# Kernel tuning notes

Hardware: AMD Instinct MI355X
Metric: run time of the kernel (lower is better)

The kernel has to match this reference:

```python
import jax, jax.numpy as jnp
import numpy as np

N_HEADS = 16


def setup_inputs() -> dict:
    key = jax.random.key(0)
    ks = jax.random.split(key, 7)
    B, S, D = 2, 2048, 1024
    x = jax.random.normal(ks[0], (B, S, D), dtype=jnp.float32)
    attn_mask = jax.random.normal(ks[1], (S, S), dtype=jnp.float32) * 0.1
    attn_bias = jax.random.normal(ks[2], (B, S, S), dtype=jnp.float32) * 0.1
    Wqkv = jax.random.normal(ks[3], (D, 3 * D), dtype=jnp.float32) * (D ** -0.5)
    bqkv = jnp.zeros((3 * D,), dtype=jnp.float32)
    Wout = jax.random.normal(ks[4], (D, D), dtype=jnp.float32) * (D ** -0.5)
    bout = jnp.zeros((D,), dtype=jnp.float32)
    return {"x": x, "attn_mask": attn_mask, "attn_bias": attn_bias,
            "Wqkv": Wqkv, "bqkv": bqkv, "Wout": Wout, "bout": bout}


def reference(x, attn_mask, attn_bias, Wqkv, bqkv, Wout, bout):
    B, S, D = x.shape
    H = N_HEADS
    hd = D // H
    # qkv projection: [B,S,3D] -> [3,B,H,S,hd]
    qkv = (x @ Wqkv + bqkv).reshape(B, S, 3, H, hd).transpose(2, 0, 3, 1, 4)
    q, k, v = qkv[0], qkv[1], qkv[2]
    scores = jnp.einsum('bhqd,bhkd->bhqk', q, k) / (hd ** 0.5)
    scores = scores + attn_mask[None, None, :, :] + attn_bias[:, None, :, :]
    attn = jax.nn.softmax(scores, axis=-1)  # dropout p=0.0 (eval)
    out = jnp.einsum('bhqk,bhkd->bhqd', attn, v)
    out = out.transpose(0, 2, 1, 3).reshape(B, S, D)
    return out @ Wout + bout
```

## Files before the change

### kernel.cpp

```cpp
#include <hip/hip_runtime.h>
#include <hip/hip_bf16.h>


#define S_LEN 2048
#define DMODEL 1024
#define NH 16
#define HD 64

typedef __bf16 bf16x8 __attribute__((ext_vector_type(8)));
typedef __bf16 bf16x4 __attribute__((ext_vector_type(4)));
typedef __bf16 bf16x2v __attribute__((ext_vector_type(2)));
typedef float f32x4 __attribute__((ext_vector_type(4)));
typedef short s16x4 __attribute__((ext_vector_type(4)));

#define GLD_LDS16(g, l)                                              \
  __builtin_amdgcn_global_load_lds(                                  \
      (const __attribute__((address_space(1))) unsigned int*)(g),    \
      (__attribute__((address_space(3))) unsigned int*)(l), 16, 0, 0)

#if __has_builtin(__builtin_amdgcn_mfma_f32_16x16x16bf16_1k)
#define HAVE_MFMA_16x16x16_BF16 1
#else
#define HAVE_MFMA_16x16x16_BF16 0
#endif

#if __has_builtin(__builtin_amdgcn_exp2f)
#define EXP2F(x) __builtin_amdgcn_exp2f(x)
#else
static __device__ __forceinline__ float EXP2F(float x) {
  float r;
  asm volatile("v_exp_f32 %0, %1" : "=v"(r) : "v"(x));
  return r;
}
#endif

#define LOG2E 1.44269504f

__global__ __launch_bounds__(256) void cvt_x(const float* __restrict__ X,
                                             __bf16* __restrict__ Xb) {
  int i = blockIdx.x * 256 + threadIdx.x;
  float4 v = ((const float4*)X)[i];
  bf16x4 o = {(__bf16)v.x, (__bf16)v.y, (__bf16)v.z, (__bf16)v.w};
  *(bf16x4*)&Xb[(size_t)i * 4] = o;
}

__global__ __launch_bounds__(256) void cvt_wt(const float* __restrict__ W,
                                              __bf16* __restrict__ Wt,
                                              int ncols) {
  __shared__ float tile[64][65];
  const int n0 = blockIdx.x * 64;
  const int k0 = blockIdx.y * 64;
  const int tid = threadIdx.x;
  {
    int c = tid & 63, r4 = tid >> 6;
#pragma unroll
    for (int p = 0; p < 16; ++p) {
      int r = r4 + p * 4;
      tile[r][c] = W[(size_t)(k0 + r) * ncols + n0 + c];
    }
  }
  __syncthreads();
  {
    int cc = (tid & 31) * 2, r8 = tid >> 5;
#pragma unroll
    for (int p = 0; p < 8; ++p) {
      int rr = r8 + p * 8;
      bf16x2v o = {(__bf16)tile[cc][rr], (__bf16)tile[cc + 1][rr]};
      *(bf16x2v*)&Wt[(size_t)(n0 + rr) * 1024 + k0 + cc] = o;
    }
  }
}

__global__ __launch_bounds__(256) void mb_fuse(const float* __restrict__ mask,
                                               const float* __restrict__ bias,
                                               __bf16* __restrict__ MB) {
  const int kt = blockIdx.x, qt = blockIdx.y, b = blockIdx.z;
  const int tid = threadIdx.x;
  __shared__ __bf16 sm[64][68];
  {
    const int r0 = tid >> 4;
    const int cc = (tid & 15) * 4;
    const float* mrow = mask + (size_t)(qt * 64) * S_LEN + kt * 64;
    const float* brow =
        bias + ((size_t)b * S_LEN + qt * 64) * S_LEN + kt * 64;
#pragma unroll
    for (int p = 0; p < 4; ++p) {
      int r = r0 + p * 16;
      float4 m = *(const float4*)(mrow + (size_t)r * S_LEN + cc);
      float4 a = *(const float4*)(brow + (size_t)r * S_LEN + cc);
      sm[r][cc + 0] = (__bf16)((m.x + a.x) * LOG2E);
      sm[r][cc + 1] = (__bf16)((m.y + a.y) * LOG2E);
      sm[r][cc + 2] = (__bf16)((m.z + a.z) * LOG2E);
      sm[r][cc + 3] = (__bf16)((m.w + a.w) * LOG2E);
    }
  }
  __syncthreads();
  const int w = tid >> 6, lane = tid & 63;
  const int quad = lane >> 4, cl = lane & 15;
  __bf16 vals[16];
#pragma unroll
  for (int ct = 0; ct < 4; ++ct) {
    bf16x4 v = *(const bf16x4*)&sm[w * 16 + cl][ct * 16 + quad * 4];
    *(bf16x4*)&vals[ct * 4] = v;
  }
  __bf16* op =
      MB + (((size_t)(b * 32 + qt) * 32 + kt) * 4096) + (w * 64 + lane) * 16;
  *(bf16x8*)op = *(bf16x8*)&vals[0];
  *(bf16x8*)(op + 8) = *(bf16x8*)&vals[8];
}

__global__ __launch_bounds__(256) void gemm_qkv_mfma(
    const __bf16* __restrict__ Xb, const __bf16* __restrict__ Wt,
    const float* __restrict__ bqkv, __bf16* __restrict__ Qb,
    __bf16* __restrict__ Kb, __bf16* __restrict__ Vtb) {
  __shared__ __align__(16) __bf16 As[128 * 32];
  __shared__ __align__(16) __bf16 Bs[128 * 32];
  const int tid = threadIdx.x;
  const int w = tid >> 6, lane = tid & 63;
  const int c = lane & 15, quad = lane >> 4;
  const int wm = w >> 1, wn = w & 1;
  const int rowBase = blockIdx.y * 128;
  const int colBase = blockIdx.x * 128;

  f32x4 acc[4][4] = {};

  const __bf16* gA0 =
      Xb + (size_t)(rowBase + w * 32 + (lane >> 2)) * 1024 + (lane & 3) * 8;
  const __bf16* gB0 =
      Wt + (size_t)(colBase + w * 32 + (lane >> 2)) * 1024 + (lane & 3) * 8;
  __bf16* lA0 = &As[(w * 32) * 32];
  __bf16* lB0 = &Bs[(w * 32) * 32];

  for (int k0 = 0; k0 < 1024; k0 += 32) {
    __syncthreads();
#pragma unroll
    for (int p = 0; p < 2; ++p) {
      GLD_LDS16(gA0 + (size_t)p * 16 * 1024 + k0, lA0 + p * 16 * 32);
      GLD_LDS16(gB0 + (size_t)p * 16 * 1024 + k0, lB0 + p * 16 * 32);
    }
    __syncthreads();

    bf16x8 af[4], bfr[4];
#pragma unroll
    for (int mt = 0; mt < 4; ++mt)
      af[mt] = *(const bf16x8*)&As[(wm * 64 + mt * 16 + c) * 32 + quad * 8];
#pragma unroll
    for (int nt = 0; nt < 4; ++nt)
      bfr[nt] = *(const bf16x8*)&Bs[(wn * 64 + nt * 16 + c) * 32 + quad * 8];
#pragma unroll
    for (int mt = 0; mt < 4; ++mt)
#pragma unroll
      for (int nt = 0; nt < 4; ++nt)
        acc[mt][nt] = __builtin_amdgcn_mfma_f32_16x16x32_bf16(
            af[mt], bfr[nt], acc[mt][nt], 0, 0, 0);
  }

#pragma unroll
  for (int mt = 0; mt < 4; ++mt) {
    int row0 = rowBase + wm * 64 + mt * 16 + quad * 4;
#pragma unroll
    for (int nt = 0; nt < 4; ++nt) {
      int col = colBase + wn * 64 + nt * 16 + c;
      float bias = bqkv[col];
      int three = col >> 10;
      int h = (col & 1023) >> 6;
      int d = col & 63;
#pragma unroll
      for (int r = 0; r < 4; ++r) {
        int rr = row0 + r;
        int bb = rr >> 11, s = rr & 2047;
        float val = acc[mt][nt][r] + bias;
        size_t ho = (size_t)(bb * NH + h);
        if (three == 0)
          Qb[(ho * S_LEN + s) * HD + d] = (__bf16)val;
        else if (three == 1)
          Kb[(ho * S_LEN + s) * HD + d] = (__bf16)val;
        else
          Vtb[(ho * HD + d) * S_LEN + s] = (__bf16)val;
      }
    }
  }
}

__global__ __launch_bounds__(256) void attn_mfma(
    const __bf16* __restrict__ Qb, const __bf16* __restrict__ Kb,
    const __bf16* __restrict__ Vtb, const __bf16* __restrict__ MB,
    __bf16* __restrict__ AOb) {
  const int qt = blockIdx.x, h = blockIdx.y, b = blockIdx.z;
  const int tid = threadIdx.x;
  const int w = tid >> 6;
  const int lane = tid & 63;
  const int c = lane & 15;
  const int quad = lane >> 4;

  __shared__ __align__(16) __bf16 Ks[2][64 * 64];
  __shared__ __align__(16) __bf16 Vs[2][64 * 64];
#if !HAVE_MFMA_16x16x16_BF16
  __shared__ __align__(16) __bf16 P2[4][16 * 72];
#endif

  const size_t headoff = (size_t)(b * NH + h) * S_LEN * HD;
  const __bf16* Qg = Qb + headoff + (size_t)(qt * 128) * HD;
  const __bf16* Kg = Kb + headoff;
  const __bf16* Vg = Vtb + headoff;
  const __bf16* MBq0 =
      MB + ((size_t)(b * 32 + qt * 2 + 0) * 32) * 4096 + (w * 64 + lane) * 16;
  const __bf16* MBq1 =
      MB + ((size_t)(b * 32 + qt * 2 + 1) * 32) * 4096 + (w * 64 + lane) * 16;

  const int f0 = tid >> 3, f1 = f0 + 32;
  const int j = tid & 7;
  const int sj0 = j ^ (f0 & 7);
  const int sj1 = j ^ (f1 & 7);
  const int lds0 = tid * 8;
  const int lds1 = (256 + tid) * 8;

  bf16x8 qa[2][2];
#pragma unroll
  for (int g = 0; g < 2; ++g) {
    qa[g][0] = *(const bf16x8*)(Qg + (g * 64 + w * 16 + c) * HD + quad * 8);
    qa[g][1] =
        *(const bf16x8*)(Qg + (g * 64 + w * 16 + c) * HD + quad * 8 + 32);
  }

  const int rs0 = (quad ^ (c & 7)) * 8;
  const int rs1 = ((quad + 4) ^ (c & 7)) * 8;

  f32x4 Oa[2][4] = {};
  f32x4 psum[2] = {};

  GLD_LDS16(Kg + (size_t)f0 * HD + sj0 * 8, &Ks[0][lds0]);
  GLD_LDS16(Kg + (size_t)f1 * HD + sj1 * 8, &Ks[0][lds1]);
  GLD_LDS16(Vg + (size_t)f0 * S_LEN + sj0 * 8, &Vs[0][lds0]);
  GLD_LDS16(Vg + (size_t)f1 * S_LEN + sj1 * 8, &Vs[0][lds1]);

  const __bf16* kgp0 = Kg + (size_t)(64 + f0) * HD + sj0 * 8;
  const __bf16* kgp1 = Kg + (size_t)(64 + f1) * HD + sj1 * 8;
  const __bf16* vgp0 = Vg + (size_t)f0 * S_LEN + 64 + sj0 * 8;
  const __bf16* vgp1 = Vg + (size_t)f1 * S_LEN + 64 + sj1 * 8;

  bf16x8 rMB[2][2];
  rMB[0][0] = *(const bf16x8*)MBq0;
  rMB[0][1] = *(const bf16x8*)(MBq0 + 8);
  rMB[1][0] = *(const bf16x8*)MBq1;
  rMB[1][1] = *(const bf16x8*)(MBq1 + 8);

  __syncthreads();

  const float c1 = 0.125f * LOG2E;

#pragma unroll 2
  for (int kt = 0; kt < 32; ++kt) {
    const int cur = kt & 1, nxt = cur ^ 1;
    bf16x8 nMB[2][2];
    {
      const __bf16* m0 = MBq0 + (size_t)(kt + 1) * 4096;
      const __bf16* m1 = MBq1 + (size_t)(kt + 1) * 4096;
      nMB[0][0] = *(const bf16x8*)m0;
      nMB[0][1] = *(const bf16x8*)(m0 + 8);
      nMB[1][0] = *(const bf16x8*)m1;
      nMB[1][1] = *(const bf16x8*)(m1 + 8);
    }
    if (kt < 31) {
      GLD_LDS16(kgp0, &Ks[nxt][lds0]);
      GLD_LDS16(kgp1, &Ks[nxt][lds1]);
      GLD_LDS16(vgp0, &Vs[nxt][lds0]);
      GLD_LDS16(vgp1, &Vs[nxt][lds1]);
    }
    kgp0 += 64 * HD;
    kgp1 += 64 * HD;
    vgp0 += 64;
    vgp1 += 64;

    bf16x8 kf0[4], kf1[4];
#pragma unroll
    for (int ct = 0; ct < 4; ++ct) {
      kf0[ct] = *(const bf16x8*)&Ks[cur][(ct * 16 + c) * 64 + rs0];
      kf1[ct] = *(const bf16x8*)&Ks[cur][(ct * 16 + c) * 64 + rs1];
    }

    f32x4 sv[2][4];
    __builtin_amdgcn_s_setprio(1);
#pragma unroll
    for (int g = 0; g < 2; ++g)
#pragma unroll
      for (int ct = 0; ct < 4; ++ct) {
        f32x4 a = {};
        a = __builtin_amdgcn_mfma_f32_16x16x32_bf16(kf0[ct], qa[g][0], a, 0,
                                                    0, 0);
        a = __builtin_amdgcn_mfma_f32_16x16x32_bf16(kf1[ct], qa[g][1], a, 0,
                                                    0, 0);
        sv[g][ct] = a;
      }
    __builtin_amdgcn_s_setprio(0);

#if HAVE_MFMA_16x16x16_BF16
    s16x4 vf[4][4];
#pragma unroll
    for (int ft = 0; ft < 4; ++ft) {
      const int fr = ft * 16 + c;
#pragma unroll
      for (int ct = 0; ct < 4; ++ct) {
        const int chunk = ((ct * 2 + (quad >> 1)) ^ (fr & 7)) * 8 +
                          (quad & 1) * 4;
        vf[ft][ct] = *(const s16x4*)&Vs[cur][fr * 64 + chunk];
      }
    }
#endif

    s16x4 pb[2][4];
#pragma unroll
    for (int g = 0; g < 2; ++g)
#pragma unroll
      for (int ct = 0; ct < 4; ++ct) {
        f32x4 pv;
#pragma unroll
        for (int r = 0; r < 4; ++r) {
          float mb = (ct < 2) ? (float)rMB[g][0][ct * 4 + r]
                              : (float)rMB[g][1][(ct - 2) * 4 + r];
          pv[r] = EXP2F(sv[g][ct][r] * c1 + mb);
        }
        psum[g] += pv;
        __bf16 t4[4];
#pragma unroll
        for (int r = 0; r < 4; ++r) t4[r] = (__bf16)pv[r];
        pb[g][ct] = *(s16x4*)t4;
      }
#pragma unroll
    for (int g = 0; g < 2; ++g) {
      rMB[g][0] = nMB[g][0];
      rMB[g][1] = nMB[g][1];
    }

#if HAVE_MFMA_16x16x16_BF16
    __builtin_amdgcn_s_setprio(1);
#pragma unroll
    for (int g = 0; g < 2; ++g)
#pragma unroll
      for (int ft = 0; ft < 4; ++ft)
#pragma unroll
        for (int ct = 0; ct < 4; ++ct)
          Oa[g][ft] = __builtin_amdgcn_mfma_f32_16x16x16bf16_1k(
              vf[ft][ct], pb[g][ct], Oa[g][ft], 0, 0, 0);
    __builtin_amdgcn_s_setprio(0);
#else
#pragma unroll
    for (int g = 0; g < 2; ++g) {
#pragma unroll
      for (int ct = 0; ct < 4; ++ct)
        *(bf16x4*)&P2[w][c * 72 + ct * 16 + quad * 4] = *(bf16x4*)&pb[g][ct];
      bf16x8 pf0 = *(const bf16x8*)&P2[w][c * 72 + quad * 8];
      bf16x8 pf1 = *(const bf16x8*)&P2[w][c * 72 + 32 + quad * 8];
#pragma unroll
      for (int ft = 0; ft < 4; ++ft) {
        const int fr = ft * 16 + c;
        bf16x8 vf0 = *(const bf16x8*)&Vs[cur][fr * 64 + rs0];
        bf16x8 vf1 = *(const bf16x8*)&Vs[cur][fr * 64 + rs1];
        Oa[g][ft] = __builtin_amdgcn_mfma_f32_16x16x32_bf16(vf0, pf0,
                                                            Oa[g][ft], 0, 0, 0);
        Oa[g][ft] = __builtin_amdgcn_mfma_f32_16x16x32_bf16(vf1, pf1,
                                                            Oa[g][ft], 0, 0, 0);
      }
    }
#endif

    __syncthreads();
  }
#pragma unroll
  for (int g = 0; g < 2; ++g) {
    float lsum = psum[g][0] + psum[g][1] + psum[g][2] + psum[g][3];
    lsum += __shfl_xor(lsum, 16);
    lsum += __shfl_xor(lsum, 32);
    const float invl = 1.0f / lsum;
    __bf16* orow = AOb +
                   (size_t)(b * S_LEN + qt * 128 + g * 64 + w * 16 + c) *
                       DMODEL +
                   h * HD;
#pragma unroll
    for (int ft = 0; ft < 4; ++ft) {
      __bf16 t4[4];
#pragma unroll
      for (int r = 0; r < 4; ++r) t4[r] = (__bf16)(Oa[g][ft][r] * invl);
      *(bf16x4*)(orow + ft * 16 + quad * 4) = *(bf16x4*)t4;
    }
  }
}

__global__ __launch_bounds__(256) void gemm_out_mfma(
    const __bf16* __restrict__ AOb, const __bf16* __restrict__ Wt2,
    const float* __restrict__ bout, float* __restrict__ Out) {
  __shared__ __align__(16) __bf16 As[128 * 32];
  __shared__ __align__(16) __bf16 Bs[64 * 32];
  const int tid = threadIdx.x;
  const int w = tid >> 6, lane = tid & 63;
  const int c = lane & 15, quad = lane >> 4;
  const int rowBase = blockIdx.y * 128;
  const int colBase = blockIdx.x * 64;

  f32x4 acc[2][4] = {};

  const __bf16* gA0 =
      AOb + (size_t)(rowBase + w * 32 + (lane >> 2)) * 1024 + (lane & 3) * 8;
  const __bf16* gB0 =
      Wt2 + (size_t)(colBase + w * 16 + (lane >> 2)) * 1024 + (lane & 3) * 8;
  __bf16* lA0 = &As[(w * 32) * 32];
  __bf16* lB0 = &Bs[(w * 16) * 32];

  for (int k0 = 0; k0 < 1024; k0 += 32) {
    __syncthreads();
#pragma unroll
    for (int p = 0; p < 2; ++p)
      GLD_LDS16(gA0 + (size_t)p * 16 * 1024 + k0, lA0 + p * 16 * 32);
    GLD_LDS16(gB0 + k0, lB0);
    __syncthreads();

    bf16x8 af[2], bfr[4];
#pragma unroll
    for (int mt = 0; mt < 2; ++mt)
      af[mt] = *(const bf16x8*)&As[(w * 32 + mt * 16 + c) * 32 + quad * 8];
#pragma unroll
    for (int nt = 0; nt < 4; ++nt)
      bfr[nt] = *(const bf16x8*)&Bs[(nt * 16 + c) * 32 + quad * 8];
#pragma unroll
    for (int mt = 0; mt < 2; ++mt)
#pragma unroll
      for (int nt = 0; nt < 4; ++nt)
        acc[mt][nt] = __builtin_amdgcn_mfma_f32_16x16x32_bf16(
            af[mt], bfr[nt], acc[mt][nt], 0, 0, 0);
  }

#pragma unroll
  for (int mt = 0; mt < 2; ++mt) {
    int row0 = rowBase + w * 32 + mt * 16 + quad * 4;
#pragma unroll
    for (int nt = 0; nt < 4; ++nt) {
      int col = colBase + nt * 16 + c;
      float bias = bout[col];
#pragma unroll
      for (int r = 0; r < 4; ++r)
        Out[(size_t)(row0 + r) * 1024 + col] = acc[mt][nt][r] + bias;
    }
  }
}

extern "C" void kernel_launch(void* const* d_in, const int* in_sizes, int n_in,
                              void* d_out, int out_size, void* d_ws,
                              size_t ws_size, hipStream_t stream) {
  const float* x = (const float*)d_in[0];
  const float* attn_mask = (const float*)d_in[1];
  const float* attn_bias = (const float*)d_in[2];
  const float* Wqkv = (const float*)d_in[3];
  const float* bqkv = (const float*)d_in[4];
  const float* Wout = (const float*)d_in[5];
  const float* bout = (const float*)d_in[6];
  float* out = (float*)d_out;

  __bf16* base = (__bf16*)d_ws;
  __bf16* Xb = base;
  __bf16* AOb = base;
  __bf16* Wt = base + 4194304;
  __bf16* Qb = base + 8388608;
  __bf16* Kb = base + 12582912;
  __bf16* Vtb = base + 16777216;
  __bf16* MB = base + 20971520;
  __bf16* Wt2 = base + 29360128;

  cvt_x<<<4096, 256, 0, stream>>>(x, Xb);
  cvt_wt<<<dim3(48, 16), 256, 0, stream>>>(Wqkv, Wt, 3072);
  cvt_wt<<<dim3(16, 16), 256, 0, stream>>>(Wout, Wt2, 1024);
  mb_fuse<<<dim3(32, 32, 2), 256, 0, stream>>>(attn_mask, attn_bias, MB);
  gemm_qkv_mfma<<<dim3(24, 32), 256, 0, stream>>>(Xb, Wt, bqkv, Qb, Kb, Vtb);
  attn_mfma<<<dim3(16, NH, 2), 256, 0, stream>>>(Qb, Kb, Vtb, MB, AOb);
  gemm_out_mfma<<<dim3(16, 32), 256, 0, stream>>>(AOb, Wt2, bout, out);
}
```

Baseline: 273.3 us.

## Split attention key range across two blocks and merge preprocessing launches

The attention kernel now splits the 32 key tiles into two halves handled by separate blocks. This doubles the grid so more of the GPU's compute units are occupied. Each half writes unnormalized bf16 partial outputs and row sums, and a new combine kernel adds the halves and normalizes them. Separately, the conversion kernels for x, both weights and mask+bias are fused into one preprocess launch to cut launch overhead. The split adds an extra global round trip for the partial outputs. It also reuses workspace regions and the output buffer as scratch.

```diff
diff --git a/kernel.cpp b/kernel.cpp
--- a/kernel.cpp
+++ b/kernel.cpp
@@ -36,77 +36,88 @@
 
 #define LOG2E 1.44269504f
 
-__global__ __launch_bounds__(256) void cvt_x(const float* __restrict__ X,
-                                             __bf16* __restrict__ Xb) {
-  int i = blockIdx.x * 256 + threadIdx.x;
-  float4 v = ((const float4*)X)[i];
-  bf16x4 o = {(__bf16)v.x, (__bf16)v.y, (__bf16)v.z, (__bf16)v.w};
-  *(bf16x4*)&Xb[(size_t)i * 4] = o;
-}
-
-__global__ __launch_bounds__(256) void cvt_wt(const float* __restrict__ W,
-                                              __bf16* __restrict__ Wt,
-                                              int ncols) {
-  __shared__ float tile[64][65];
-  const int n0 = blockIdx.x * 64;
-  const int k0 = blockIdx.y * 64;
+__global__ __launch_bounds__(256) void preprocess(
+    const float* __restrict__ x, const float* __restrict__ mask,
+    const float* __restrict__ bias, const float* __restrict__ Wqkv,
+    const float* __restrict__ Wout, __bf16* __restrict__ Xb,
+    __bf16* __restrict__ Wt, __bf16* __restrict__ Wt2,
+    __bf16* __restrict__ MB) {
+  __shared__ __align__(16) char smem[64 * 65 * 4];
+  const int bid = blockIdx.x;
   const int tid = threadIdx.x;
-  {
-    int c = tid & 63, r4 = tid >> 6;
-#pragma unroll
-    for (int p = 0; p < 16; ++p) {
-      int r = r4 + p * 4;
-      tile[r][c] = W[(size_t)(k0 + r) * ncols + n0 + c];
-    }
-  }
-  __syncthreads();
-  {
-    int cc = (tid & 31) * 2, r8 = tid >> 5;
-#pragma unroll
-    for (int p = 0; p < 8; ++p) {
-      int rr = r8 + p * 8;
-      bf16x2v o = {(__bf16)tile[cc][rr], (__bf16)tile[cc + 1][rr]};
-      *(bf16x2v*)&Wt[(size_t)(n0 + rr) * 1024 + k0 + cc] = o;
-    }
-  }
-}
-
-__global__ __launch_bounds__(256) void mb_fuse(const float* __restrict__ mask,
-                                               const float* __restrict__ bias,
-                                               __bf16* __restrict__ MB) {
-  const int kt = blockIdx.x, qt = blockIdx.y, b = blockIdx.z;
-  const int tid = threadIdx.x;
-  __shared__ __bf16 sm[64][68];
-  {
-    const int r0 = tid >> 4;
-    const int cc = (tid & 15) * 4;
-    const float* mrow = mask + (size_t)(qt * 64) * S_LEN + kt * 64;
-    const float* brow =
-        bias + ((size_t)b * S_LEN + qt * 64) * S_LEN + kt * 64;
-#pragma unroll
-    for (int p = 0; p < 4; ++p) {
-      int r = r0 + p * 16;
-      float4 m = *(const float4*)(mrow + (size_t)r * S_LEN + cc);
-      float4 a = *(const float4*)(brow + (size_t)r * S_LEN + cc);
-      sm[r][cc + 0] = (__bf16)((m.x + a.x) * LOG2E);
-      sm[r][cc + 1] = (__bf16)((m.y + a.y) * LOG2E);
-      sm[r][cc + 2] = (__bf16)((m.z + a.z) * LOG2E);
-      sm[r][cc + 3] = (__bf16)((m.w + a.w) * LOG2E);
-    }
-  }
-  __syncthreads();
-  const int w = tid >> 6, lane = tid & 63;
-  const int quad = lane >> 4, cl = lane & 15;
-  __bf16 vals[16];
-#pragma unroll
-  for (int ct = 0; ct < 4; ++ct) {
-    bf16x4 v = *(const bf16x4*)&sm[w * 16 + cl][ct * 16 + quad * 4];
-    *(bf16x4*)&vals[ct * 4] = v;
-  }
-  __bf16* op =
-      MB + (((size_t)(b * 32 + qt) * 32 + kt) * 4096) + (w * 64 + lane) * 16;
-  *(bf16x8*)op = *(bf16x8*)&vals[0];
-  *(bf16x8*)(op + 8) = *(bf16x8*)&vals[8];
+
+  if (bid < 4096) {
+    int i = bid * 256 + tid;
+    float4 v = ((const float4*)x)[i];
+    bf16x4 o = {(__bf16)v.x, (__bf16)v.y, (__bf16)v.z, (__bf16)v.w};
+    *(bf16x4*)&Xb[(size_t)i * 4] = o;
+  } else if (bid < 5120) {
+    const float* W;
+    __bf16* Wo;
+    int ncols, n0, k0;
+    if (bid < 4864) {
+      int id = bid - 4096;
+      W = Wqkv; Wo = Wt; ncols = 3072;
+      n0 = (id % 48) * 64; k0 = (id / 48) * 64;
+    } else {
+      int id = bid - 4864;
+      W = Wout; Wo = Wt2; ncols = 1024;
+      n0 = (id & 15) * 64; k0 = (id >> 4) * 64;
+    }
+    float(*tile)[65] = (float(*)[65])smem;
+    {
+      int c = tid & 63, r4 = tid >> 6;
+#pragma unroll
+      for (int p = 0; p < 16; ++p) {
+        int r = r4 + p * 4;
+        tile[r][c] = W[(size_t)(k0 + r) * ncols + n0 + c];
+      }
+    }
+    __syncthreads();
+    {
+      int cc = (tid & 31) * 2, r8 = tid >> 5;
+#pragma unroll
+      for (int p = 0; p < 8; ++p) {
+        int rr = r8 + p * 8;
+        bf16x2v o = {(__bf16)tile[cc][rr], (__bf16)tile[cc + 1][rr]};
+        *(bf16x2v*)&Wo[(size_t)(n0 + rr) * 1024 + k0 + cc] = o;
+      }
+    }
+  } else {
+    int id = bid - 5120;
+    const int kt = id & 31, qt = (id >> 5) & 31, b = id >> 10;
+    __bf16(*sm)[68] = (__bf16(*)[68])smem;
+    {
+      const int r0 = tid >> 4;
+      const int cc = (tid & 15) * 4;
+      const float* mrow = mask + (size_t)(qt * 64) * S_LEN + kt * 64;
+      const float* brow =
+          bias + ((size_t)b * S_LEN + qt * 64) * S_LEN + kt * 64;
+#pragma unroll
+      for (int p = 0; p < 4; ++p) {
+        int r = r0 + p * 16;
+        float4 m = *(const float4*)(mrow + (size_t)r * S_LEN + cc);
+        float4 a = *(const float4*)(brow + (size_t)r * S_LEN + cc);
+        sm[r][cc + 0] = (__bf16)((m.x + a.x) * LOG2E);
+        sm[r][cc + 1] = (__bf16)((m.y + a.y) * LOG2E);
+        sm[r][cc + 2] = (__bf16)((m.z + a.z) * LOG2E);
+        sm[r][cc + 3] = (__bf16)((m.w + a.w) * LOG2E);
+      }
+    }
+    __syncthreads();
+    const int w = tid >> 6, lane = tid & 63;
+    const int quad = lane >> 4, cl = lane & 15;
+    __bf16 vals[16];
+#pragma unroll
+    for (int ct = 0; ct < 4; ++ct) {
+      bf16x4 v = *(const bf16x4*)&sm[w * 16 + cl][ct * 16 + quad * 4];
+      *(bf16x4*)&vals[ct * 4] = v;
+    }
+    __bf16* op =
+        MB + (((size_t)(b * 32 + qt) * 32 + kt) * 4096) + (w * 64 + lane) * 16;
+    *(bf16x8*)op = *(bf16x8*)&vals[0];
+    *(bf16x8*)(op + 8) = *(bf16x8*)&vals[8];
+  }
 }
 
 __global__ __launch_bounds__(256) void gemm_qkv_mfma(
@@ -185,8 +196,10 @@
 __global__ __launch_bounds__(256) void attn_mfma(
     const __bf16* __restrict__ Qb, const __bf16* __restrict__ Kb,
     const __bf16* __restrict__ Vtb, const __bf16* __restrict__ MB,
-    __bf16* __restrict__ AOb) {
-  const int qt = blockIdx.x, h = blockIdx.y, b = blockIdx.z;
+    __bf16* __restrict__ PO, float* __restrict__ L) {
+  const int qt = blockIdx.x, h = blockIdx.y;
+  const int b = blockIdx.z >> 1, half = blockIdx.z & 1;
+  const int kt0 = half * 16;
   const int tid = threadIdx.x;
   const int w = tid >> 6;
   const int lane = tid & 63;
@@ -203,10 +216,13 @@
   const __bf16* Qg = Qb + headoff + (size_t)(qt * 128) * HD;
   const __bf16* Kg = Kb + headoff;
   const __bf16* Vg = Vtb + headoff;
-  const __bf16* MBq0 =
-      MB + ((size_t)(b * 32 + qt * 2 + 0) * 32) * 4096 + (w * 64 + lane) * 16;
-  const __bf16* MBq1 =
-      MB + ((size_t)(b * 32 + qt * 2 + 1) * 32) * 4096 + (w * 64 + lane) * 16;
+  const __bf16* MBq0 = MB + ((size_t)(b * 32 + qt * 2 + 0) * 32 + kt0) * 4096 +
+                       (w * 64 + lane) * 16;
+  const __bf16* MBq1 = MB + ((size_t)(b * 32 + qt * 2 + 1) * 32 + kt0) * 4096 +
+                       (w * 64 + lane) * 16;
+
+  __bf16* POx = PO + (size_t)half * 4194304;
+  float* Lx = L + half * 65536;
 
   const int f0 = tid >> 3, f1 = f0 + 32;
   const int j = tid & 7;
@@ -229,15 +245,16 @@
   f32x4 Oa[2][4] = {};
   f32x4 psum[2] = {};
 
-  GLD_LDS16(Kg + (size_t)f0 * HD + sj0 * 8, &Ks[0][lds0]);
-  GLD_LDS16(Kg + (size_t)f1 * HD + sj1 * 8, &Ks[0][lds1]);
-  GLD_LDS16(Vg + (size_t)f0 * S_LEN + sj0 * 8, &Vs[0][lds0]);
-  GLD_LDS16(Vg + (size_t)f1 * S_LEN + sj1 * 8, &Vs[0][lds1]);
-
-  const __bf16* kgp0 = Kg + (size_t)(64 + f0) * HD + sj0 * 8;
-  const __bf16* kgp1 = Kg + (size_t)(64 + f1) * HD + sj1 * 8;
-  const __bf16* vgp0 = Vg + (size_t)f0 * S_LEN + 64 + sj0 * 8;
-  const __bf16* vgp1 = Vg + (size_t)f1 * S_LEN + 64 + sj1 * 8;
+  const int kb0 = kt0 * 64;
+  GLD_LDS16(Kg + (size_t)(kb0 + f0) * HD + sj0 * 8, &Ks[0][lds0]);
+  GLD_LDS16(Kg + (size_t)(kb0 + f1) * HD + sj1 * 8, &Ks[0][lds1]);
+  GLD_LDS16(Vg + (size_t)f0 * S_LEN + kb0 + sj0 * 8, &Vs[0][lds0]);
+  GLD_LDS16(Vg + (size_t)f1 * S_LEN + kb0 + sj1 * 8, &Vs[0][lds1]);
+
+  const __bf16* kgp0 = Kg + (size_t)(kb0 + 64 + f0) * HD + sj0 * 8;
+  const __bf16* kgp1 = Kg + (size_t)(kb0 + 64 + f1) * HD + sj1 * 8;
+  const __bf16* vgp0 = Vg + (size_t)f0 * S_LEN + kb0 + 64 + sj0 * 8;
+  const __bf16* vgp1 = Vg + (size_t)f1 * S_LEN + kb0 + 64 + sj1 * 8;
 
   bf16x8 rMB[2][2];
   rMB[0][0] = *(const bf16x8*)MBq0;
@@ -250,18 +267,18 @@
   const float c1 = 0.125f * LOG2E;
 
 #pragma unroll 2
-  for (int kt = 0; kt < 32; ++kt) {
-    const int cur = kt & 1, nxt = cur ^ 1;
+  for (int lkt = 0; lkt < 16; ++lkt) {
+    const int cur = lkt & 1, nxt = cur ^ 1;
     bf16x8 nMB[2][2];
     {
-      const __bf16* m0 = MBq0 + (size_t)(kt + 1) * 4096;
-      const __bf16* m1 = MBq1 + (size_t)(kt + 1) * 4096;
+      const __bf16* m0 = MBq0 + (size_t)(lkt + 1) * 4096;
+      const __bf16* m1 = MBq1 + (size_t)(lkt + 1) * 4096;
       nMB[0][0] = *(const bf16x8*)m0;
       nMB[0][1] = *(const bf16x8*)(m0 + 8);
       nMB[1][0] = *(const bf16x8*)m1;
       nMB[1][1] = *(const bf16x8*)(m1 + 8);
     }
-    if (kt < 31) {
+    if (lkt < 15) {
       GLD_LDS16(kgp0, &Ks[nxt][lds0]);
       GLD_LDS16(kgp1, &Ks[nxt][lds1]);
       GLD_LDS16(vgp0, &Vs[nxt][lds0]);
@@ -371,8 +388,9 @@
     float lsum = psum[g][0] + psum[g][1] + psum[g][2] + psum[g][3];
     lsum += __shfl_xor(lsum, 16);
     lsum += __shfl_xor(lsum, 32);
-    const float invl = 1.0f / lsum;
-    __bf16* orow = AOb +
+    if (lane < 16)
+      Lx[(size_t)(b * NH + h) * S_LEN + qt * 128 + g * 64 + w * 16 + c] = lsum;
+    __bf16* orow = POx +
                    (size_t)(b * S_LEN + qt * 128 + g * 64 + w * 16 + c) *
                        DMODEL +
                    h * HD;
@@ -380,10 +398,29 @@
     for (int ft = 0; ft < 4; ++ft) {
       __bf16 t4[4];
 #pragma unroll
-      for (int r = 0; r < 4; ++r) t4[r] = (__bf16)(Oa[g][ft][r] * invl);
+      for (int r = 0; r < 4; ++r) t4[r] = (__bf16)Oa[g][ft][r];
       *(bf16x4*)(orow + ft * 16 + quad * 4) = *(bf16x4*)t4;
     }
   }
+}
+
+__global__ __launch_bounds__(256) void combine(const __bf16* __restrict__ PO,
+                                               const float* __restrict__ L,
+                                               __bf16* __restrict__ AOb) {
+  const int i = blockIdx.x * 256 + threadIdx.x;
+  const size_t e = (size_t)i * 8;
+  const int hidx = (int)(e >> 6) & 15;
+  const int s = (int)(e >> 10) & 2047;
+  const int b = (int)(e >> 21);
+  const size_t li = ((size_t)(b * NH + hidx) << 11) + s;
+  const float invl = 1.0f / (L[li] + L[65536 + li]);
+  bf16x8 a = *(const bf16x8*)&PO[e];
+  bf16x8 c = *(const bf16x8*)&PO[4194304 + e];
+  __bf16 o[8];
+#pragma unroll
+  for (int k = 0; k < 8; ++k)
+    o[k] = (__bf16)(((float)a[k] + (float)c[k]) * invl);
+  *(bf16x8*)&AOb[e] = *(bf16x8*)o;
 }
 
 __global__ __launch_bounds__(256) void gemm_out_mfma(
@@ -457,19 +494,20 @@
 
   __bf16* base = (__bf16*)d_ws;
   __bf16* Xb = base;
-  __bf16* AOb = base;
+  __bf16* PO = base;
   __bf16* Wt = base + 4194304;
   __bf16* Qb = base + 8388608;
   __bf16* Kb = base + 12582912;
   __bf16* Vtb = base + 16777216;
+  __bf16* AOb = base + 16777216;
   __bf16* MB = base + 20971520;
   __bf16* Wt2 = base + 29360128;
-
-  cvt_x<<<4096, 256, 0, stream>>>(x, Xb);
-  cvt_wt<<<dim3(48, 16), 256, 0, stream>>>(Wqkv, Wt, 3072);
-  cvt_wt<<<dim3(16, 16), 256, 0, stream>>>(Wout, Wt2, 1024);
-  mb_fuse<<<dim3(32, 32, 2), 256, 0, stream>>>(attn_mask, attn_bias, MB);
+  float* Lf = (float*)d_out;
+
+  preprocess<<<7168, 256, 0, stream>>>(x, attn_mask, attn_bias, Wqkv, Wout,
+                                       Xb, Wt, Wt2, MB);
   gemm_qkv_mfma<<<dim3(24, 32), 256, 0, stream>>>(Xb, Wt, bqkv, Qb, Kb, Vtb);
-  attn_mfma<<<dim3(16, NH, 2), 256, 0, stream>>>(Qb, Kb, Vtb, MB, AOb);
+  attn_mfma<<<dim3(16, NH, 4), 256, 0, stream>>>(Qb, Kb, Vtb, MB, PO, Lf);
+  combine<<<2048, 256, 0, stream>>>(PO, Lf, AOb);
   gemm_out_mfma<<<dim3(16, 32), 256, 0, stream>>>(AOb, Wt2, bout, out);
 }
```

Measured after the change: 278.4 us. No clear change (+1.9%).
